# Performance work log

Hardware: AMD Instinct MI355X
Metric: run time of the kernel (lower is better)

The kernel has to match this reference:

```python
import jax, jax.numpy as jnp
import numpy as np

B_, C_, H_, W_ = 8, 128, 64, 64
OUT_ = 128
D_MODEL = C_ // 4        # 32, per-chunk channels fed to Mamba
D_STATE = 16
D_CONV = 4
D_INNER = 2 * D_MODEL    # expand=2 -> 64
DT_RANK = max(1, -(-D_MODEL // 16))  # ceil(32/16)=2
SE_RED = 2


def _ln(x, g, b):
    m = x.mean(-1, keepdims=True)
    v = jnp.var(x, axis=-1, keepdims=True)
    return (x - m) / jnp.sqrt(v + 1e-5) * g + b


def _mamba(u, in_W, conv_W, conv_b, xproj_W, dt_W, dt_b, A_log, D_p, out_W):
    # u: (B, L, d_model)
    Bsz, L, _ = u.shape
    xz = u @ in_W.T                                   # (B,L,2*d_inner)
    x, z = jnp.split(xz, 2, axis=-1)
    # causal depthwise conv1d along L
    xc = jnp.swapaxes(x, 1, 2)                        # (B,d_inner,L)
    xc = jax.lax.conv_general_dilated(
        xc, conv_W, (1,), [(D_CONV - 1, 0)],
        feature_group_count=D_INNER,
        dimension_numbers=('NCH', 'OIH', 'NCH'))
    x = jax.nn.silu(jnp.swapaxes(xc + conv_b[None, :, None], 1, 2))
    x_dbl = x @ xproj_W.T                             # (B,L,dt_rank+2*d_state)
    dt, Bm, Cm = jnp.split(x_dbl, [DT_RANK, DT_RANK + D_STATE], axis=-1)
    dt = jax.nn.softplus(dt @ dt_W.T + dt_b)          # (B,L,d_inner)
    A = -jnp.exp(A_log)                               # (d_inner,d_state)
    dA = jnp.exp(dt[..., None] * A)                   # (B,L,d_inner,d_state)
    dBu = dt[..., None] * Bm[:, :, None, :] * x[..., None]

    def step(h, inp):
        dA_t, dBu_t, C_t = inp
        h = dA_t * h + dBu_t                          # (B,d_inner,d_state)
        return h, jnp.einsum('bds,bs->bd', h, C_t)

    h0 = jnp.zeros((Bsz, D_INNER, D_STATE), dtype=x.dtype)
    _, ys = jax.lax.scan(step, h0, (jnp.swapaxes(dA, 0, 1), jnp.swapaxes(dBu, 0, 1), jnp.swapaxes(Cm, 0, 1)))
    y = jnp.swapaxes(ys, 0, 1) + x * D_p
    y = y * jax.nn.silu(z)
    return y @ out_W.T


def _branch(xi, skip_scale, se_W1, se_W2, mp):
    M1 = _mamba(xi, *mp)                              # (B,L,c)
    M2 = skip_scale * xi
    # SE: adaptive avg-pool over spatial == mean over tokens; cat over channels
    y = jnp.concatenate([M1, M2], axis=-1).mean(axis=1)   # (B,2c)
    y = jax.nn.sigmoid(jax.nn.relu(y @ se_W1.T) @ se_W2.T)
    g1, g2 = jnp.split(y, 2, axis=-1)
    return g1[:, None, :] * M1 + g2[:, None, :] * M2


def _pvm(x, norm_g, norm_b, proj_W, proj_b, skip_scale, se_W1, se_W2,
         in_W, conv_W, conv_b, xproj_W, dt_W, dt_b, A_log, D_p, out_W):
    B, C, H, W = x.shape
    L = H * W
    xf = jnp.swapaxes(x.reshape(B, C, L), 1, 2)       # (B,L,C)
    xn = _ln(xf, norm_g, norm_b)
    mp = (in_W, conv_W, conv_b, xproj_W, dt_W, dt_b, A_log, D_p, out_W)
    outs = [_branch(c, skip_scale, se_W1, se_W2, mp) for c in jnp.split(xn, 4, axis=2)]
    xm = jnp.concatenate(outs, axis=2)                # (B,L,C)
    xm = _ln(xm, norm_g, norm_b)
    xm = xm @ proj_W.T + proj_b                       # (B,L,out)
    return jnp.swapaxes(xm, 1, 2).reshape(B, proj_W.shape[0], H, W)


def setup_inputs():
    key = jax.random.key(0)
    ks = jax.random.split(key, 10)
    p = {}
    p['x'] = jax.random.normal(ks[0], (B_, C_, H_, W_), jnp.float32)
    p['norm_g'] = jnp.ones((C_,), jnp.float32)
    p['norm_b'] = jnp.zeros((C_,), jnp.float32)
    p['proj_W'] = jax.random.normal(ks[1], (OUT_, C_), jnp.float32) * 0.05
    p['proj_b'] = jnp.zeros((OUT_,), jnp.float32)
    p['skip_scale'] = jnp.ones((1,), jnp.float32)
    p['se_W1'] = jax.random.normal(ks[2], (SE_RED, 2 * D_MODEL), jnp.float32) * 0.1
    p['se_W2'] = jax.random.normal(ks[3], (2 * D_MODEL, SE_RED), jnp.float32) * 0.1
    p['in_W'] = jax.random.normal(ks[4], (2 * D_INNER, D_MODEL), jnp.float32) * 0.1
    p['conv_W'] = jax.random.normal(ks[5], (D_INNER, 1, D_CONV), jnp.float32) * 0.2
    p['conv_b'] = jnp.zeros((D_INNER,), jnp.float32)
    p['xproj_W'] = jax.random.normal(ks[6], (DT_RANK + 2 * D_STATE, D_INNER), jnp.float32) * 0.1
    p['dt_W'] = jax.random.normal(ks[7], (D_INNER, DT_RANK), jnp.float32) * 0.1
    p['dt_b'] = jnp.full((D_INNER,), -4.6, jnp.float32)  # softplus(-4.6) ~ 0.01 init dt
    p['A_log'] = jnp.log(jnp.broadcast_to(jnp.arange(1.0, D_STATE + 1.0, dtype=jnp.float32), (D_INNER, D_STATE)))
    p['D_p'] = jnp.ones((D_INNER,), jnp.float32)
    p['out_W'] = jax.random.normal(ks[8], (D_MODEL, D_INNER), jnp.float32) * 0.1
    return p


def reference(x, norm_g, norm_b, proj_W, proj_b, skip_scale, se_W1, se_W2,
              in_W, conv_W, conv_b, xproj_W, dt_W, dt_b, A_log, D_p, out_W):
    return _pvm(x, norm_g, norm_b, proj_W, proj_b, skip_scale, se_W1, se_W2,
                in_W, conv_W, conv_b, xproj_W, dt_W, dt_b, A_log, D_p, out_W)
```

## Files before the change

### kernel.cpp

```cpp
#include <hip/hip_runtime.h>
#include <math.h>

typedef _Float16 h16;

#define DEV static __device__ __forceinline__

constexpr int B_ = 8, C_ = 128, L_ = 4096, OUT_ = 128;
constexpr int NCH = 4, DM = 32, DS = 16, DI = 64;
constexpr int NI = 32;
constexpr int NSEG = 128;
constexpr int SL = L_ / NSEG;

DEV float sigmoidf_(float x) { return 1.f / (1.f + __expf(-x)); }
DEV float siluf_(float x) { return x * sigmoidf_(x); }
DEV float softplusf_(float x) { return (x > 20.f) ? x : __logf(1.f + __expf(x)); }

template <int CTRL>
DEV float dpp_add_(float x) {
  int v = __builtin_amdgcn_update_dpp(0, __float_as_int(x), CTRL, 0xf, 0xf, false);
  return x + __int_as_float(v);
}

typedef __attribute__((ext_vector_type(8))) _Float16 f16x8;
typedef __attribute__((ext_vector_type(4))) _Float16 f16x4;
typedef __attribute__((ext_vector_type(4))) float f32x4;

DEV void powladder_(float E, float* out) {
  float E2 = E * E;
  float E4 = E2 * E2;
  float E8 = E4 * E4;
  float E3 = E2 * E;
  out[0] = E;       out[1] = E2;      out[2] = E3;      out[3] = E4;
  out[4] = E4 * E;  out[5] = E4 * E2; out[6] = E4 * E3; out[7] = E8;
  out[8] = E8 * E;  out[9] = E8 * E2; out[10] = E8 * E3; out[11] = E8 * E4;
  out[12] = E8 * out[4]; out[13] = E8 * out[5]; out[14] = E8 * out[6];
  out[15] = E8 * E8;
}

DEV void powladder8_(float E, float* out) {
  float E2 = E * E, E3 = E2 * E, E4 = E2 * E2;
  out[0] = E; out[1] = E2; out[2] = E3; out[3] = E4;
  out[4] = E4 * E; out[5] = E4 * E2; out[6] = E4 * E3; out[7] = E4 * E4;
}

__global__ __launch_bounds__(256) void k0_wcvt(
    const float* __restrict__ in_W, const float* __restrict__ xproj_W,
    const float* __restrict__ out_W, const float* __restrict__ proj_W,
    const float* __restrict__ A_log, h16* __restrict__ WH,
    float* __restrict__ AVT, float* __restrict__ Zp) {
  int tid = blockIdx.x * 256 + threadIdx.x;
  if (tid < 3072) Zp[tid] = 0.f;
  if (tid < 1024) AVT[tid] = -__expf(A_log[tid]);
  if (tid < 4096) {
    WH[tid] = (h16)in_W[tid];
  } else if (tid < 7168) {
    int j = tid - 4096;
    int r = j >> 6;
    WH[tid] = (r < 34) ? (h16)xproj_W[r * 64 + (j & 63)] : (h16)0.f;
  } else if (tid < 9216) {
    WH[tid] = (h16)out_W[tid - 7168];
  } else if (tid < 25600) {
    WH[tid] = (h16)proj_W[tid - 9216];
  }
}

__global__ __launch_bounds__(256) void k1_ln(const float* __restrict__ x,
                                             const float* __restrict__ gn,
                                             const float* __restrict__ bn,
                                             h16* __restrict__ XNH,
                                             float* __restrict__ SUMXN) {
  int bid = blockIdx.x;
  int b = bid >> 6, tile = bid & 63;
  int t0 = tile * 64;
  int tid = threadIdx.x;
  __shared__ float xT[128][65];
  __shared__ float gnS[128], bnS[128];
  __shared__ float red[256];
  if (tid < 128) { gnS[tid] = gn[tid]; bnS[tid] = bn[tid]; }
  for (int k = tid; k < 8192; k += 256) {
    int c = k >> 6, tt = k & 63;
    xT[c][tt] = x[((size_t)(b * C_ + c)) * L_ + t0 + tt];
  }
  __syncthreads();
  {
    int tok = tid >> 2, q = tid & 3;
    float s = 0.f, qq = 0.f;
#pragma unroll
    for (int j = 0; j < 32; ++j) {
      float v = xT[q + 4 * j][tok];
      s += v; qq += v * v;
    }
    s = dpp_add_<0xB1>(s); qq = dpp_add_<0xB1>(qq);
    s = dpp_add_<0x4E>(s); qq = dpp_add_<0x4E>(qq);
    float m = s * (1.f / 128.f);
    float var = qq * (1.f / 128.f) - m * m;
    float rs = rsqrtf(var + 1e-5f);
#pragma unroll
    for (int j = 0; j < 32; ++j) {
      int c = q + 4 * j;
      float v = xT[c][tok];
      xT[c][tok] = (v - m) * rs * gnS[c] + bnS[c];
    }
  }
  __syncthreads();
  float acc = 0.f;
  int cfix = tid & 127;
  for (int k = tid; k < 8192; k += 256) {
    int tt = k >> 7, c = k & 127;
    acc += xT[c][tt];
  }
  for (int k = tid; k < 1024; k += 256) {
    int tt = k >> 4, c8 = (k & 15) * 8;
    f16x8 hv;
#pragma unroll
    for (int j = 0; j < 8; ++j) hv[j] = (_Float16)xT[c8 + j][tt];
    *(f16x8*)&XNH[((size_t)(b * L_ + t0 + tt)) * C_ + c8] = hv;
  }
  red[tid] = acc;
  __syncthreads();
  if (tid < 128) atomicAdd(&SUMXN[b * C_ + cfix], red[tid] + red[tid + 128]);
}

__global__ __launch_bounds__(256) void k2_prep(
    const h16* __restrict__ WH, const float* __restrict__ conv_W,
    const float* __restrict__ conv_b, const float* __restrict__ dt_W,
    const float* __restrict__ dt_b, const float* __restrict__ AVT,
    const h16* __restrict__ XNH, h16* __restrict__ SX2, h16* __restrict__ SDT2,
    h16* __restrict__ SB2, h16* __restrict__ SC2, h16* __restrict__ SZ2,
    float* __restrict__ Pp, float* __restrict__ Qp) {
  int bid = blockIdx.x;
  int i = bid >> 6, tile = bid & 63;
  int b = i >> 2, ch = i & 3;
  int t0 = tile * 64;
  int tid = threadIdx.x;
  int w = __builtin_amdgcn_readfirstlane(tid >> 6);
  int lane = tid & 63;

  __shared__ __attribute__((aligned(16))) union {
    _Float16 uH[80][40];
    float xdS[64][36];
    _Float16 zL[64][72];
  } U;
  __shared__ __attribute__((aligned(16))) _Float16 preH[68][68];
  __shared__ __attribute__((aligned(16))) _Float16 xH[64][72];
  __shared__ float convWS[64][4];
  __shared__ float dtWS[64][2];
  __shared__ float dtbS[64], cbS[64];

  convWS[tid >> 2][tid & 3] = conv_W[tid];
  if (tid < 128) dtWS[tid >> 1][tid & 1] = dt_W[tid];
  if (tid < 64) { dtbS[tid] = dt_b[tid]; cbS[tid] = conv_b[tid]; }
  const h16* xnh = XNH + (size_t)b * L_ * C_ + ch * DM;
  for (int k = tid; k < 320; k += 256) {
    int r = k >> 2, c8 = (k & 3) * 8;
    int tg = t0 - 3 + r;
    f16x8 v = {0, 0, 0, 0, 0, 0, 0, 0};
    if (r < 67 && tg >= 0) v = *(const f16x8*)&xnh[(size_t)tg * C_ + c8];
    *(f16x8*)&U.uH[r][c8] = v;
  }
  __syncthreads();

  int rsel = lane & 15, ksel = (lane >> 4) * 8;
  {
    int nt = w;
    f16x8 bf = *(const f16x8*)&WH[(size_t)(nt * 16 + rsel) * 32 + ksel];
    int row0q = (lane >> 4) << 2;
    int col = nt * 16 + rsel;
#pragma unroll
    for (int mt = 0; mt < 5; ++mt) {
      f16x8 af = *(const f16x8*)&U.uH[mt * 16 + rsel][ksel];
      f32x4 acc = {0.f, 0.f, 0.f, 0.f};
      acc = __builtin_amdgcn_mfma_f32_16x16x32_f16(af, bf, acc, 0, 0, 0);
      int row0 = mt * 16 + row0q;
#pragma unroll
      for (int r = 0; r < 4; ++r) {
        int row = row0 + r;
        if (row < 67) preH[row][col] = (_Float16)acc[r];
      }
    }
  }
  f32x4 zacc[4];
  {
    f16x8 bf = *(const f16x8*)&U.uH[3 + w * 16 + rsel][ksel];
#pragma unroll
    for (int mt = 0; mt < 4; ++mt) {
      f16x8 af = *(const f16x8*)&WH[(size_t)(64 + mt * 16 + rsel) * 32 + ksel];
      f32x4 acc = {0.f, 0.f, 0.f, 0.f};
      zacc[mt] = __builtin_amdgcn_mfma_f32_16x16x32_f16(af, bf, acc, 0, 0, 0);
    }
  }
  __syncthreads();

  h16* SXp = SX2 + ((size_t)i * L_ + t0) * DI;
  for (int k = tid; k < 4096; k += 256) {
    int r = k >> 6, d = k & 63;
    float v = cbS[d];
#pragma unroll
    for (int j = 0; j < 4; ++j) v = fmaf(convWS[d][j], (float)preH[r + j][d], v);
    v = siluf_(v);
    xH[r][d] = (_Float16)v;
    SXp[(size_t)r * DI + d] = (h16)v;
  }
  __syncthreads();

  {
    int mt = w;
    f16x8 a0 = *(const f16x8*)&xH[mt * 16 + rsel][ksel];
    f16x8 a1 = *(const f16x8*)&xH[mt * 16 + rsel][32 + ksel];
    int row0 = mt * 16 + ((lane >> 4) << 2);
#pragma unroll
    for (int nt = 0; nt < 3; ++nt) {
      const h16* wp = WH + 4096 + (size_t)(nt * 16 + rsel) * 64;
      f16x8 b0 = *(const f16x8*)&wp[ksel];
      f16x8 b1 = *(const f16x8*)&wp[32 + ksel];
      f32x4 acc = {0.f, 0.f, 0.f, 0.f};
      acc = __builtin_amdgcn_mfma_f32_16x16x32_f16(a0, b0, acc, 0, 0, 0);
      acc = __builtin_amdgcn_mfma_f32_16x16x32_f16(a1, b1, acc, 0, 0, 0);
      int col = nt * 16 + rsel;
      if (col < 34) {
#pragma unroll
        for (int r = 0; r < 4; ++r) U.xdS[row0 + r][col] = acc[r];
      }
    }
  }
  __syncthreads();

  h16* dtL = (h16*)&preH[0][0];
  h16* SDTp = SDT2 + ((size_t)i * L_ + t0) * DI;
  for (int k = tid; k < 4096; k += 256) {
    int d = k & 63, r = k >> 6;
    float raw = fmaf(U.xdS[r][0], dtWS[d][0], fmaf(U.xdS[r][1], dtWS[d][1], dtbS[d]));
    float dtv = softplusf_(raw);
    dtL[r * 68 + d] = (_Float16)dtv;
    SDTp[(size_t)r * DI + d] = (h16)dtv;
  }
  h16* SBp = SB2 + ((size_t)i * L_ + t0) * DS;
  h16* SCp = SC2 + ((size_t)i * L_ + t0) * DS;
  for (int k = tid; k < 1024; k += 256) {
    int s = k & 15, r = k >> 4;
    SBp[(size_t)r * DS + s] = (h16)U.xdS[r][2 + s];
    SCp[(size_t)r * DS + s] = (h16)U.xdS[r][18 + s];
  }
  __syncthreads();

  {
    int seg = w >> 1, shalf = w & 1;
    int s0 = shalf * 8;
    float Av[16];
    {
      const float* avp = AVT + lane * 16;
#pragma unroll
      for (int j = 0; j < 4; ++j) *(float4*)&Av[4 * j] = *(const float4*)(avp + 4 * j);
    }
    float A0 = Av[0];
    bool okf = true;
#pragma unroll
    for (int s = 0; s < 16; ++s)
      okf &= fabsf(Av[s] - (float)(s + 1) * A0) <= 1e-4f * fabsf(Av[s]);
    int fastp = __all(okf ? 1 : 0);
    float h[8];
#pragma unroll
    for (int j = 0; j < 8; ++j) h[j] = 0.f;
    float sdt = 0.f;
    int rowbase = seg * SL;
    for (int t = 0; t < SL; ++t) {
      int row = rowbase + t;
      float dt = (float)dtL[row * 68 + lane];
      float xv = (float)xH[row][lane];
      float dtx = dt * xv;
      float dA[8];
      if (fastp) {
        powladder8_(__expf(A0 * dt), dA);
        if (shalf) {
          float E8 = dA[7];
#pragma unroll
          for (int j = 0; j < 8; ++j) dA[j] *= E8;
        }
      } else {
#pragma unroll
        for (int j = 0; j < 8; ++j) dA[j] = __expf(Av[s0 + j] * dt);
      }
      const float* brow = &U.xdS[row][2 + s0];
#pragma unroll
      for (int j = 0; j < 8; ++j) h[j] = fmaf(dA[j], h[j], dtx * brow[j]);
      sdt += dt;
    }
    float P[8];
    if (fastp) {
      powladder8_(__expf(A0 * sdt), P);
      if (shalf) {
        float E8 = P[7];
#pragma unroll
        for (int j = 0; j < 8; ++j) P[j] *= E8;
      }
    } else {
#pragma unroll
      for (int j = 0; j < 8; ++j) P[j] = __expf(Av[s0 + j] * sdt);
    }
    int segg = tile * 2 + seg;
    size_t base = (((size_t)i * NSEG + segg) * DI + lane) * DS + s0;
    *(float4*)(Pp + base) = *(float4*)&P[0];
    *(float4*)(Pp + base + 4) = *(float4*)&P[4];
    *(float4*)(Qp + base) = *(float4*)&h[0];
    *(float4*)(Qp + base + 4) = *(float4*)&h[4];
  }
  __syncthreads();

  {
    int tok = w * 16 + rsel;
    int zq = (lane >> 4) << 2;
#pragma unroll
    for (int mt = 0; mt < 4; ++mt) {
      f16x4 pk;
#pragma unroll
      for (int r = 0; r < 4; ++r) pk[r] = (_Float16)siluf_(zacc[mt][r]);
      *(f16x4*)&U.zL[tok][mt * 16 + zq] = pk;
    }
  }
  __syncthreads();
  h16* SZp = SZ2 + ((size_t)i * L_ + t0) * DI;
  for (int k = tid; k < 512; k += 256) {
    int r = k >> 3, dblk = (k & 7) * 8;
    f16x8 v = *(const f16x8*)&U.zL[r][dblk];
    *(f16x8*)&SZp[(size_t)r * DI + dblk] = v;
  }
}

__global__ __launch_bounds__(64) void k3b_comb(float* __restrict__ Pp,
                                               const float* __restrict__ Qp) {
  int g = blockIdx.x * 64 + threadIdx.x;
  int ds = g & 1023;
  int i = g >> 10;
  size_t base = (size_t)i * NSEG * DI * DS + ds;
  constexpr int SST = DI * DS;
  float H = 0.f;
  for (int sb = 0; sb < NSEG; sb += 16) {
    float Pv[16], Qv[16];
#pragma unroll
    for (int j = 0; j < 16; ++j) {
      size_t a = base + (size_t)(sb + j) * SST;
      Pv[j] = Pp[a];
      Qv[j] = Qp[a];
    }
#pragma unroll
    for (int j = 0; j < 16; ++j) {
      size_t a = base + (size_t)(sb + j) * SST;
      Pp[a] = H;
      H = fmaf(Pv[j], H, Qv[j]);
    }
  }
}

__global__ __launch_bounds__(256) void k3c_scan(
    const float* __restrict__ AVT, const h16* __restrict__ SDT2,
    const h16* __restrict__ SX2, const h16* __restrict__ SB2,
    const h16* __restrict__ SC2, const h16* __restrict__ SZ2,
    const float* __restrict__ D_p, const float* __restrict__ H0p,
    h16* __restrict__ YS2, float* __restrict__ SUMYF) {
  int bid = blockIdx.x;
  int i = bid >> 5, sg = bid & 31;
  int tid = threadIdx.x;
  int w = tid >> 6, lane = tid & 63;
  int seg = sg * 4 + w;
  int t0 = seg * SL;
  __shared__ float rowS[4][SL][36];
  {
    int tk = lane & 31, hf = lane >> 5;
    const h16* p = (hf ? SC2 : SB2) + ((size_t)i * L_ + t0 + tk) * DS;
    float4 r0 = *(const float4*)p;
    float4 r1 = *(const float4*)(p + 8);
    const h16* hp0 = (const h16*)&r0;
    const h16* hp1 = (const h16*)&r1;
#pragma unroll
    for (int s = 0; s < 8; ++s) {
      rowS[w][tk][hf * 16 + s] = (float)hp0[s];
      rowS[w][tk][hf * 16 + 8 + s] = (float)hp1[s];
    }
  }
  __syncthreads();
  float Av[16];
  {
    const float* avp = AVT + lane * 16;
#pragma unroll
    for (int j = 0; j < 4; ++j) *(float4*)&Av[4 * j] = *(const float4*)(avp + 4 * j);
  }
  float A0 = Av[0];
  bool okf = true;
#pragma unroll
  for (int s = 0; s < 16; ++s) okf &= fabsf(Av[s] - (float)(s + 1) * A0) <= 1e-4f * fabsf(Av[s]);
  int fastp = __all(okf ? 1 : 0);
  float Dp = D_p[lane];
  float h[16];
  {
    size_t base = (((size_t)i * NSEG + seg) * DI + lane) * DS;
#pragma unroll
    for (int j = 0; j < 4; ++j) *(float4*)&h[4 * j] = *(const float4*)(H0p + base + 4 * j);
  }
  const h16* pdt = SDT2 + ((size_t)i * L_ + t0) * DI + lane;
  const h16* pxx = SX2 + ((size_t)i * L_ + t0) * DI + lane;
  const h16* pzz = SZ2 + ((size_t)i * L_ + t0) * DI + lane;
  h16* pys = YS2 + ((size_t)i * L_ + t0) * DI + lane;
  float dtc = (float)pdt[0], xvc = (float)pxx[0], zvc = (float)pzz[0];
  float sum = 0.f;
  for (int t = 0; t < SL; ++t) {
    float dt = dtc, xv = xvc, zv = zvc;
    if (t < SL - 1) {
      dtc = (float)pdt[(t + 1) * DI];
      xvc = (float)pxx[(t + 1) * DI];
      zvc = (float)pzz[(t + 1) * DI];
    }
    const float* row = &rowS[w][t][0];
    float Bv[16], Cv[16];
#pragma unroll
    for (int j = 0; j < 4; ++j) {
      *(float4*)&Bv[4 * j] = *(const float4*)(row + 4 * j);
      *(float4*)&Cv[4 * j] = *(const float4*)(row + 16 + 4 * j);
    }
    float dtx = dt * xv;
    float dA[16];
    if (fastp) {
      powladder_(__expf(A0 * dt), dA);
    } else {
#pragma unroll
      for (int s = 0; s < 16; ++s) dA[s] = __expf(Av[s] * dt);
    }
    float y0 = 0.f, y1 = 0.f, y2 = 0.f, y3 = 0.f;
#pragma unroll
    for (int s = 0; s < 16; s += 4) {
      h[s] = fmaf(dA[s], h[s], dtx * Bv[s]);       y0 = fmaf(h[s], Cv[s], y0);
      h[s + 1] = fmaf(dA[s + 1], h[s + 1], dtx * Bv[s + 1]); y1 = fmaf(h[s + 1], Cv[s + 1], y1);
      h[s + 2] = fmaf(dA[s + 2], h[s + 2], dtx * Bv[s + 2]); y2 = fmaf(h[s + 2], Cv[s + 2], y2);
      h[s + 3] = fmaf(dA[s + 3], h[s + 3], dtx * Bv[s + 3]); y3 = fmaf(h[s + 3], Cv[s + 3], y3);
    }
    float y = (y0 + y1) + (y2 + y3);
    float yf = fmaf(xv, Dp, y) * zv;
    pys[(size_t)t * DI] = (h16)yf;
    sum += yf;
  }
  atomicAdd(&SUMYF[i * DI + lane], sum);
}

__global__ __launch_bounds__(256) void k56_comb_proj(
    const float* __restrict__ out_W, const float* __restrict__ skip_p,
    const float* __restrict__ se_W1, const float* __restrict__ se_W2,
    const float* __restrict__ SUMYF, const float* __restrict__ SUMXN,
    const h16* __restrict__ YS2, const float* __restrict__ gn,
    const float* __restrict__ bn, const h16* __restrict__ WH,
    const float* __restrict__ proj_b, const h16* __restrict__ XNH,
    float* __restrict__ out) {
  int bid = blockIdx.x;
  int b = bid >> 6, tile = bid & 63;
  int t0 = tile * 64;
  int tid = threadIdx.x;
  int w = __builtin_amdgcn_readfirstlane(tid >> 6);
  int lane = tid & 63;
  __shared__ __attribute__((aligned(16))) union {
    float xmS[64][132];
    _Float16 projH[64][136];
  } U;
  __shared__ __attribute__((aligned(16))) union {
    struct {
      _Float16 yH[64][72];
      _Float16 owH[32][72];
    } pre;
    _Float16 xmH[64][136];
  } V;
  __shared__ float gAll[4][64];
  __shared__ float gnS[128], bnS[128];
  float* catS = (float*)&V.pre.yH[0][0];
  float* seL = catS + 256;

  if (tid < 128) { gnS[tid] = gn[tid]; bnS[tid] = bn[tid]; }
  for (int k = tid; k < 256; k += 256) {
    int r = k >> 3, c8 = (k & 7) * 8;
    *(f16x8*)&V.pre.owH[r][c8] = *(const f16x8*)&WH[7168 + r * 64 + c8];
  }
  const h16* xmh = XNH + (size_t)b * L_ * C_;
  for (int k = tid; k < 1024; k += 256) {
    int tt = k >> 4, c8 = (k & 15) * 8;
    f16x8 hv = *(const f16x8*)&xmh[(size_t)(t0 + tt) * C_ + c8];
#pragma unroll
    for (int j = 0; j < 8; ++j) U.xmS[tt][c8 + j] = (float)hv[j];
  }
  {
    int ch = tid >> 6, j = tid & 63;
    float invL = 1.f / (float)L_;
    if (j < 32) {
      const float* sy = SUMYF + (b * 4 + ch) * DI;
      const float* ow = out_W + j * 64;
      float acc = 0.f;
#pragma unroll
      for (int dd = 0; dd < 64; ++dd) acc = fmaf(sy[dd], ow[dd], acc);
      catS[ch * 64 + j] = acc * invL;
    } else {
      catS[ch * 64 + j] = skip_p[0] * SUMXN[b * C_ + ch * DM + (j - 32)] * invL;
    }
  }
  __syncthreads();
  if (tid < 8) {
    int ch = tid >> 1, r = tid & 1;
    float acc = 0.f;
#pragma unroll
    for (int k = 0; k < 64; ++k) acc = fmaf(catS[ch * 64 + k], se_W1[r * 64 + k], acc);
    seL[tid] = fmaxf(acc, 0.f);
  }
  __syncthreads();
  {
    int ch = tid >> 6, j = tid & 63;
    gAll[ch][j] = sigmoidf_(fmaf(seL[ch * 2], se_W2[j * 2], seL[ch * 2 + 1] * se_W2[j * 2 + 1]));
  }
  __syncthreads();

  int rsel = lane & 15, ksel = (lane >> 4) * 8;
  float skip = skip_p[0];
  for (int ch = 0; ch < 4; ++ch) {
    const h16* py = YS2 + ((size_t)(b * 4 + ch) * L_ + t0) * DI;
    for (int k = tid; k < 512; k += 256) {
      int tt = k >> 3, dblk = (k & 7) * 8;
      *(f16x8*)&V.pre.yH[tt][dblk] = *(const f16x8*)&py[(size_t)tt * DI + dblk];
    }
    __syncthreads();
    f16x8 a0 = *(const f16x8*)&V.pre.yH[w * 16 + rsel][ksel];
    f16x8 a1 = *(const f16x8*)&V.pre.yH[w * 16 + rsel][32 + ksel];
    int row0 = w * 16 + ((lane >> 4) << 2);
#pragma unroll
    for (int nt = 0; nt < 2; ++nt) {
      f16x8 b0 = *(const f16x8*)&V.pre.owH[nt * 16 + rsel][ksel];
      f16x8 b1 = *(const f16x8*)&V.pre.owH[nt * 16 + rsel][32 + ksel];
      f32x4 acc = {0.f, 0.f, 0.f, 0.f};
      acc = __builtin_amdgcn_mfma_f32_16x16x32_f16(a0, b0, acc, 0, 0, 0);
      acc = __builtin_amdgcn_mfma_f32_16x16x32_f16(a1, b1, acc, 0, 0, 0);
      int o = nt * 16 + rsel;
      float g1 = gAll[ch][o], g2s = gAll[ch][32 + o] * skip;
      int cc = ch * 32 + o;
#pragma unroll
      for (int r = 0; r < 4; ++r) {
        int tok = row0 + r;
        U.xmS[tok][cc] = g1 * acc[r] + g2s * U.xmS[tok][cc];
      }
    }
    __syncthreads();
  }

  {
    int tok = tid >> 2, q = tid & 3;
    float s = 0.f, qq = 0.f;
#pragma unroll
    for (int j = 0; j < 32; ++j) {
      float v = U.xmS[tok][4 * j + q];
      s += v; qq += v * v;
    }
    s = dpp_add_<0xB1>(s); qq = dpp_add_<0xB1>(qq);
    s = dpp_add_<0x4E>(s); qq = dpp_add_<0x4E>(qq);
    float m = s * (1.f / 128.f);
    float var = qq * (1.f / 128.f) - m * m;
    float rs = rsqrtf(var + 1e-5f);
#pragma unroll
    for (int j = 0; j < 32; ++j) {
      int c = 4 * j + q;
      float v = U.xmS[tok][c];
      U.xmS[tok][c] = (v - m) * rs * gnS[c] + bnS[c];
    }
  }
  __syncthreads();
  for (int k = tid; k < 1024; k += 256) {
    int tt = k >> 4, cblk = (k & 15) * 8;
    float4 v0 = *(const float4*)&U.xmS[tt][cblk];
    float4 v1 = *(const float4*)&U.xmS[tt][cblk + 4];
    f16x8 hv;
    hv[0] = (_Float16)v0.x; hv[1] = (_Float16)v0.y;
    hv[2] = (_Float16)v0.z; hv[3] = (_Float16)v0.w;
    hv[4] = (_Float16)v1.x; hv[5] = (_Float16)v1.y;
    hv[6] = (_Float16)v1.z; hv[7] = (_Float16)v1.w;
    *(f16x8*)&V.xmH[tt][cblk] = hv;
  }
  __syncthreads();
  f16x8 af[4];
#pragma unroll
  for (int kc = 0; kc < 4; ++kc)
    af[kc] = *(const f16x8*)&V.xmH[w * 16 + rsel][kc * 32 + ksel];
  int row0 = w * 16 + ((lane >> 4) << 2);
#pragma unroll
  for (int half = 0; half < 2; ++half) {
    for (int k = tid; k < 1024; k += 256) {
      int o = k >> 4, cblk = (k & 15) * 8;
      *(f16x8*)&U.projH[o][cblk] =
          *(const f16x8*)&WH[9216 + (half * 64 + o) * 128 + cblk];
    }
    __syncthreads();
#pragma unroll
    for (int nt = 0; nt < 4; ++nt) {
      int ol = nt * 16 + rsel;
      int o = half * 64 + ol;
      float pb = proj_b[o];
      f32x4 acc = {pb, pb, pb, pb};
#pragma unroll
      for (int kc = 0; kc < 4; ++kc) {
        f16x8 bf = *(const f16x8*)&U.projH[ol][kc * 32 + ksel];
        acc = __builtin_amdgcn_mfma_f32_16x16x32_f16(af[kc], bf, acc, 0, 0, 0);
      }
      *(float4*)&out[((size_t)(b * OUT_ + o)) * L_ + t0 + row0] =
          make_float4(acc[0], acc[1], acc[2], acc[3]);
    }
    __syncthreads();
  }
}

extern "C" void kernel_launch(void* const* d_in, const int* in_sizes, int n_in,
                              void* d_out, int out_size, void* d_ws, size_t ws_size,
                              hipStream_t stream) {
  const float* x = (const float*)d_in[0];
  const float* norm_g = (const float*)d_in[1];
  const float* norm_b = (const float*)d_in[2];
  const float* proj_W = (const float*)d_in[3];
  const float* proj_b = (const float*)d_in[4];
  const float* skip = (const float*)d_in[5];
  const float* se_W1 = (const float*)d_in[6];
  const float* se_W2 = (const float*)d_in[7];
  const float* in_W = (const float*)d_in[8];
  const float* conv_W = (const float*)d_in[9];
  const float* conv_b = (const float*)d_in[10];
  const float* xproj_W = (const float*)d_in[11];
  const float* dt_W = (const float*)d_in[12];
  const float* dt_b = (const float*)d_in[13];
  const float* A_log = (const float*)d_in[14];
  const float* D_p = (const float*)d_in[15];
  const float* out_W = (const float*)d_in[16];
  float* out = (float*)d_out;

  float* SUMYF = (float*)d_ws;
  float* SUMXN = SUMYF + NI * DI;
  float* Pp = SUMXN + B_ * C_;
  float* Qp = Pp + (size_t)NI * DI * NSEG * DS;
  h16* YS2 = (h16*)(Qp + (size_t)NI * DI * NSEG * DS);
  h16* SX2 = YS2 + (size_t)NI * L_ * DI;
  h16* SDT2 = SX2 + (size_t)NI * L_ * DI;
  h16* SB2 = SDT2 + (size_t)NI * L_ * DI;
  h16* SC2 = SB2 + (size_t)NI * L_ * DS;
  h16* SZ2 = SC2 + (size_t)NI * L_ * DS;
  h16* XNH = SZ2 + (size_t)NI * L_ * DI;
  h16* WH = XNH + (size_t)B_ * L_ * C_;
  float* AVT = (float*)(WH + 25600);

  k0_wcvt<<<112, 256, 0, stream>>>(in_W, xproj_W, out_W, proj_W, A_log, WH, AVT,
                                   SUMYF);
  k1_ln<<<B_ * 64, 256, 0, stream>>>(x, norm_g, norm_b, XNH, SUMXN);
  k2_prep<<<NI * 64, 256, 0, stream>>>(WH, conv_W, conv_b, dt_W, dt_b, AVT,
                                       XNH, SX2, SDT2, SB2, SC2, SZ2, Pp, Qp);
  k3b_comb<<<512, 64, 0, stream>>>(Pp, Qp);
  k3c_scan<<<NI * 32, 256, 0, stream>>>(AVT, SDT2, SX2, SB2, SC2, SZ2, D_p,
                                        Pp, YS2, SUMYF);
  k56_comb_proj<<<B_ * 64, 256, 0, stream>>>(out_W, skip, se_W1, se_W2, SUMYF,
                                             SUMXN, YS2, norm_g, norm_b, WH,
                                             proj_b, XNH, out);
}
```

Before: 210.3 us.

## Store segment scan carries in fp16 and fold weight conversion into LayerNorm kernel

The per-segment decay products and partial states (Pp/Qp) exchanged between the prep, combine and scan kernels are now stored in half precision instead of float, halving that intermediate traffic. The separate weight-conversion kernel is merged into the LayerNorm kernel as extra blocks, and zeroing of the accumulators becomes a memset, removing one launch. Storing scan state and decay products in fp16 risks precision loss, since decay powers can underflow and state values get rounded.

```diff
diff --git a/kernel.cpp b/kernel.cpp
--- a/kernel.cpp
+++ b/kernel.cpp
@@ -43,36 +43,33 @@
   out[4] = E4 * E; out[5] = E4 * E2; out[6] = E4 * E3; out[7] = E4 * E4;
 }
 
-__global__ __launch_bounds__(256) void k0_wcvt(
-    const float* __restrict__ in_W, const float* __restrict__ xproj_W,
-    const float* __restrict__ out_W, const float* __restrict__ proj_W,
-    const float* __restrict__ A_log, h16* __restrict__ WH,
-    float* __restrict__ AVT, float* __restrict__ Zp) {
-  int tid = blockIdx.x * 256 + threadIdx.x;
-  if (tid < 3072) Zp[tid] = 0.f;
-  if (tid < 1024) AVT[tid] = -__expf(A_log[tid]);
-  if (tid < 4096) {
-    WH[tid] = (h16)in_W[tid];
-  } else if (tid < 7168) {
-    int j = tid - 4096;
-    int r = j >> 6;
-    WH[tid] = (r < 34) ? (h16)xproj_W[r * 64 + (j & 63)] : (h16)0.f;
-  } else if (tid < 9216) {
-    WH[tid] = (h16)out_W[tid - 7168];
-  } else if (tid < 25600) {
-    WH[tid] = (h16)proj_W[tid - 9216];
-  }
-}
-
-__global__ __launch_bounds__(256) void k1_ln(const float* __restrict__ x,
-                                             const float* __restrict__ gn,
-                                             const float* __restrict__ bn,
-                                             h16* __restrict__ XNH,
-                                             float* __restrict__ SUMXN) {
+__global__ __launch_bounds__(256) void k1_ln(
+    const float* __restrict__ x, const float* __restrict__ gn,
+    const float* __restrict__ bn, const float* __restrict__ in_W,
+    const float* __restrict__ xproj_W, const float* __restrict__ out_W,
+    const float* __restrict__ proj_W, const float* __restrict__ A_log,
+    h16* __restrict__ WH, float* __restrict__ AVT, h16* __restrict__ XNH,
+    float* __restrict__ SUMXN) {
   int bid = blockIdx.x;
+  int tid = threadIdx.x;
+  if (bid >= B_ * 64) {
+    int g = (bid - B_ * 64) * 256 + tid;
+    if (g < 1024) AVT[g] = -__expf(A_log[g]);
+    if (g < 4096) {
+      WH[g] = (h16)in_W[g];
+    } else if (g < 7168) {
+      int j = g - 4096;
+      int r = j >> 6;
+      WH[g] = (r < 34) ? (h16)xproj_W[r * 64 + (j & 63)] : (h16)0.f;
+    } else if (g < 9216) {
+      WH[g] = (h16)out_W[g - 7168];
+    } else if (g < 25600) {
+      WH[g] = (h16)proj_W[g - 9216];
+    }
+    return;
+  }
   int b = bid >> 6, tile = bid & 63;
   int t0 = tile * 64;
-  int tid = threadIdx.x;
   __shared__ float xT[128][65];
   __shared__ float gnS[128], bnS[128];
   __shared__ float red[256];
@@ -127,7 +124,7 @@
     const float* __restrict__ dt_b, const float* __restrict__ AVT,
     const h16* __restrict__ XNH, h16* __restrict__ SX2, h16* __restrict__ SDT2,
     h16* __restrict__ SB2, h16* __restrict__ SC2, h16* __restrict__ SZ2,
-    float* __restrict__ Pp, float* __restrict__ Qp) {
+    h16* __restrict__ Pp, h16* __restrict__ Qp) {
   int bid = blockIdx.x;
   int i = bid >> 6, tile = bid & 63;
   int b = i >> 2, ch = i & 3;
@@ -299,10 +296,11 @@
     }
     int segg = tile * 2 + seg;
     size_t base = (((size_t)i * NSEG + segg) * DI + lane) * DS + s0;
-    *(float4*)(Pp + base) = *(float4*)&P[0];
-    *(float4*)(Pp + base + 4) = *(float4*)&P[4];
-    *(float4*)(Qp + base) = *(float4*)&h[0];
-    *(float4*)(Qp + base + 4) = *(float4*)&h[4];
+    f16x8 ph, qh;
+#pragma unroll
+    for (int j = 0; j < 8; ++j) { ph[j] = (_Float16)P[j]; qh[j] = (_Float16)h[j]; }
+    *(f16x8*)(Pp + base) = ph;
+    *(f16x8*)(Qp + base) = qh;
   }
   __syncthreads();
 
@@ -326,8 +324,8 @@
   }
 }
 
-__global__ __launch_bounds__(64) void k3b_comb(float* __restrict__ Pp,
-                                               const float* __restrict__ Qp) {
+__global__ __launch_bounds__(64) void k3b_comb(h16* __restrict__ Pp,
+                                               const h16* __restrict__ Qp) {
   int g = blockIdx.x * 64 + threadIdx.x;
   int ds = g & 1023;
   int i = g >> 10;
@@ -339,13 +337,13 @@
 #pragma unroll
     for (int j = 0; j < 16; ++j) {
       size_t a = base + (size_t)(sb + j) * SST;
-      Pv[j] = Pp[a];
-      Qv[j] = Qp[a];
+      Pv[j] = (float)Pp[a];
+      Qv[j] = (float)Qp[a];
     }
 #pragma unroll
     for (int j = 0; j < 16; ++j) {
       size_t a = base + (size_t)(sb + j) * SST;
-      Pp[a] = H;
+      Pp[a] = (h16)H;
       H = fmaf(Pv[j], H, Qv[j]);
     }
   }
@@ -355,7 +353,7 @@
     const float* __restrict__ AVT, const h16* __restrict__ SDT2,
     const h16* __restrict__ SX2, const h16* __restrict__ SB2,
     const h16* __restrict__ SC2, const h16* __restrict__ SZ2,
-    const float* __restrict__ D_p, const float* __restrict__ H0p,
+    const float* __restrict__ D_p, const h16* __restrict__ H0p,
     h16* __restrict__ YS2, float* __restrict__ SUMYF) {
   int bid = blockIdx.x;
   int i = bid >> 5, sg = bid & 31;
@@ -392,9 +390,11 @@
   float Dp = D_p[lane];
   float h[16];
   {
-    size_t base = (((size_t)i * NSEG + seg) * DI + lane) * DS;
-#pragma unroll
-    for (int j = 0; j < 4; ++j) *(float4*)&h[4 * j] = *(const float4*)(H0p + base + 4 * j);
+    const h16* hp = H0p + (((size_t)i * NSEG + seg) * DI + lane) * DS;
+    f16x8 h0a = *(const f16x8*)hp;
+    f16x8 h0b = *(const f16x8*)(hp + 8);
+#pragma unroll
+    for (int j = 0; j < 8; ++j) { h[j] = (float)h0a[j]; h[8 + j] = (float)h0b[j]; }
   }
   const h16* pdt = SDT2 + ((size_t)i * L_ + t0) * DI + lane;
   const h16* pxx = SX2 + ((size_t)i * L_ + t0) * DI + lane;
@@ -630,9 +630,9 @@
 
   float* SUMYF = (float*)d_ws;
   float* SUMXN = SUMYF + NI * DI;
-  float* Pp = SUMXN + B_ * C_;
-  float* Qp = Pp + (size_t)NI * DI * NSEG * DS;
-  h16* YS2 = (h16*)(Qp + (size_t)NI * DI * NSEG * DS);
+  h16* Pp = (h16*)(SUMXN + B_ * C_);
+  h16* Qp = Pp + (size_t)NI * DI * NSEG * DS;
+  h16* YS2 = Qp + (size_t)NI * DI * NSEG * DS;
   h16* SX2 = YS2 + (size_t)NI * L_ * DI;
   h16* SDT2 = SX2 + (size_t)NI * L_ * DI;
   h16* SB2 = SDT2 + (size_t)NI * L_ * DI;
@@ -642,9 +642,10 @@
   h16* WH = XNH + (size_t)B_ * L_ * C_;
   float* AVT = (float*)(WH + 25600);
 
-  k0_wcvt<<<112, 256, 0, stream>>>(in_W, xproj_W, out_W, proj_W, A_log, WH, AVT,
-                                   SUMYF);
-  k1_ln<<<B_ * 64, 256, 0, stream>>>(x, norm_g, norm_b, XNH, SUMXN);
+  hipMemsetAsync(SUMYF, 0, (size_t)(NI * DI + B_ * C_) * sizeof(float), stream);
+  k1_ln<<<B_ * 64 + 104, 256, 0, stream>>>(x, norm_g, norm_b, in_W, xproj_W,
+                                           out_W, proj_W, A_log, WH, AVT, XNH,
+                                           SUMXN);
   k2_prep<<<NI * 64, 256, 0, stream>>>(WH, conv_W, conv_b, dt_W, dt_b, AVT,
                                        XNH, SX2, SDT2, SB2, SC2, SZ2, Pp, Qp);
   k3b_comb<<<512, 64, 0, stream>>>(Pp, Qp);
```

Result: faster. 204.8 us (-2.6%).
